# Kernel tuning notes

Measured on AMD Instinct MI355X. Metric: run time of the kernel, lower is better.

## Reference

```python
import jax, jax.numpy as jnp
import numpy as np
from jax import lax

BATCH = 1048576
NUM_DIGITS = 10


def _build_tables():
    # Exact replication of CarryAdderCell.__init__ table construction.
    next_carry = np.zeros((200, 2), dtype=np.float32)
    digit = np.zeros((200, 10), dtype=np.float32)
    for carry in (0, 1):
        for a in range(10):
            for b in range(10):
                idx = carry * 100 + a * 10 + b
                total = a + b + carry
                next_carry[idx, total // 10] = 1.0
                digit[idx, total % 10] = 1.0
    return jnp.asarray(digit), jnp.asarray(next_carry)


def setup_inputs() -> dict:
    key = jax.random.key(0)
    ka, kb = jax.random.split(key)
    a = jax.random.randint(ka, (BATCH, NUM_DIGITS), 0, 10, dtype=jnp.int32)
    b = jax.random.randint(kb, (BATCH, NUM_DIGITS), 0, 10, dtype=jnp.int32)
    digit_table, carry_table = _build_tables()
    return {"a": a, "b": b, "digit_table": digit_table, "carry_table": carry_table}


def reference(a, b, digit_table, carry_table):
    batch = a.shape[0]

    def step(carry_idx, ab):
        a_t, b_t = ab  # [batch] each
        table_idx = carry_idx * 100 + a_t * 10 + b_t  # [batch]
        digit_logits = digit_table[table_idx]          # [batch, 10]
        h_next = carry_table[table_idx]                # [batch, 2]
        next_carry = jnp.argmax(h_next, axis=-1).astype(jnp.int32)
        return next_carry, digit_logits

    # Process least-significant digit first (pos = num_digits-1 .. 0).
    xs = (a[:, ::-1].T, b[:, ::-1].T)  # each [num_digits, batch]
    carry0 = jnp.zeros((batch,), dtype=jnp.int32)  # initial one-hot carry -> argmax 0
    final_carry, logits_lsd = lax.scan(step, carry0, xs)
    # logits_lsd: [num_digits, batch, 10] in LSD-first order -> reverse, move batch first.
    result_10 = jnp.transpose(logits_lsd[::-1], (1, 0, 2))  # [batch, num_digits, 10]
    leading = jax.nn.one_hot(final_carry, 10, dtype=digit_table.dtype)[:, None, :]
    return jnp.concatenate([leading, result_10], axis=1)  # [batch, num_digits+1, 10]
```

## Files before the change

kernel.cpp:

```cpp
#include <hip/hip_runtime.h>


#define ROWS 128
#define THREADS 256
#define FPR 110

__global__ __launch_bounds__(THREADS) void adder_onehot_kernel(
    const int* __restrict__ a, const int* __restrict__ b,
    float* __restrict__ out, int batch) {
    __shared__ uint2 packed[ROWS + 1];

    const int t = threadIdx.x;
    const int row0 = blockIdx.x * ROWS;

    if (t < ROWS && row0 + t < batch) {
        const int* ap = a + (size_t)(row0 + t) * 10;
        const int* bp = b + (size_t)(row0 + t) * 10;
        int av[10], bv[10];
#pragma unroll
        for (int p = 0; p < 10; ++p) av[p] = ap[p];
#pragma unroll
        for (int p = 0; p < 10; ++p) bv[p] = bp[p];

        int dig[11];
        int carry = 0;
#pragma unroll
        for (int p = 9; p >= 0; --p) {
            int tot = av[p] + bv[p] + carry;
            int c = tot >= 10;
            dig[1 + p] = c ? tot - 10 : tot;
            carry = c;
        }
        dig[0] = carry;

        unsigned w0 = 0, w1 = 0;
#pragma unroll
        for (int pos = 0; pos < 8; ++pos) w0 |= (unsigned)dig[pos] << (4 * pos);
#pragma unroll
        for (int pos = 8; pos < 11; ++pos) w1 |= (unsigned)dig[pos] << (4 * (pos - 8));
        packed[t] = make_uint2(w0, w1);
    }
    __syncthreads();

    const int rows_here = min(ROWS, batch - row0);
    const int total_f = rows_here * FPR;
    const int nvec = total_f >> 2;
    float4* out4 = (float4*)(out + (size_t)row0 * FPR);

    int e0 = 4 * t;
    int row = e0 / 110;
    int rem = e0 - 110 * row;

    for (int i = t; i < nvec; i += THREADS) {
        uint2 p0 = packed[row];
        uint2 p1 = packed[row + 1];
        float4 v;
        float* vp = &v.x;
#pragma unroll
        for (int k = 0; k < 4; ++k) {
            int re = rem + k;
            bool wrap = re >= 110;
            int re2 = wrap ? re - 110 : re;
            unsigned wlo = wrap ? p1.x : p0.x;
            unsigned whi = wrap ? p1.y : p0.y;
            int pos = (re2 * 205) >> 11;
            int slot = re2 - 10 * pos;
            unsigned w = (pos >= 8) ? whi : wlo;
            int digit = (w >> ((pos & 7) * 4)) & 15;
            vp[k] = (digit == slot) ? 1.0f : 0.0f;
        }
        out4[i] = v;

        row += 9;
        rem += 34;
        if (rem >= 110) { rem -= 110; ++row; }
    }

    const int tail0 = nvec * 4;
    if (t < total_f - tail0) {
        int e = tail0 + t;
        int r = e / 110;
        int re2 = e - 110 * r;
        int pos = (re2 * 205) >> 11;
        int slot = re2 - 10 * pos;
        uint2 pw = packed[r];
        unsigned w = (pos >= 8) ? pw.y : pw.x;
        int digit = (w >> ((pos & 7) * 4)) & 15;
        out[(size_t)row0 * FPR + e] = (digit == slot) ? 1.0f : 0.0f;
    }
}

extern "C" void kernel_launch(void* const* d_in, const int* in_sizes, int n_in,
                              void* d_out, int out_size, void* d_ws, size_t ws_size,
                              hipStream_t stream) {
    const int* a = (const int*)d_in[0];
    const int* b = (const int*)d_in[1];
    float* out = (float*)d_out;
    const int batch = in_sizes[0] / 10;

    const int grid = (batch + ROWS - 1) / ROWS;
    adder_onehot_kernel<<<grid, THREADS, 0, stream>>>(a, b, out, batch);
}
```

Measured before the change: 112.7 us.

## Split adder into pack kernel and store kernel via workspace

Splits the work into two kernels. The first computes the packed digit words for every row and writes them to the workspace. The second reads the packed words and emits the one-hot float output, with 256 rows per block so all threads do useful work in the load phase. It also vectorises the input loads to int2, and keeps a fused fallback for when the workspace is too small. The split adds an extra launch and a round trip of 8 bytes per row through global memory, in exchange for removing the serial compute phase in which half of each block idled before the stores.

```diff
diff --git a/kernel.cpp b/kernel.cpp
--- a/kernel.cpp
+++ b/kernel.cpp
@@ -1,48 +1,60 @@
 #include <hip/hip_runtime.h>
 
 
-#define ROWS 128
 #define THREADS 256
 #define FPR 110
 
-__global__ __launch_bounds__(THREADS) void adder_onehot_kernel(
+__device__ __forceinline__ void compute_pack(const int* __restrict__ ap,
+                                             const int* __restrict__ bp,
+                                             unsigned& w0, unsigned& w1) {
+    int av[10], bv[10];
+    const int2* ap2 = (const int2*)ap;
+    const int2* bp2 = (const int2*)bp;
+#pragma unroll
+    for (int i = 0; i < 5; ++i) {
+        int2 va = ap2[i]; av[2*i] = va.x; av[2*i+1] = va.y;
+        int2 vb = bp2[i]; bv[2*i] = vb.x; bv[2*i+1] = vb.y;
+    }
+    int dig[11];
+    int carry = 0;
+#pragma unroll
+    for (int p = 9; p >= 0; --p) {
+        int tot = av[p] + bv[p] + carry;
+        int c = tot >= 10;
+        dig[1 + p] = c ? tot - 10 : tot;
+        carry = c;
+    }
+    dig[0] = carry;
+    w0 = 0; w1 = 0;
+#pragma unroll
+    for (int pos = 0; pos < 8; ++pos) w0 |= (unsigned)dig[pos] << (4 * pos);
+#pragma unroll
+    for (int pos = 8; pos < 11; ++pos) w1 |= (unsigned)dig[pos] << (4 * (pos - 8));
+}
+
+__global__ __launch_bounds__(THREADS) void adder_pack_kernel(
     const int* __restrict__ a, const int* __restrict__ b,
-    float* __restrict__ out, int batch) {
-    __shared__ uint2 packed[ROWS + 1];
+    uint2* __restrict__ ws, int batch) {
+    int r = blockIdx.x * THREADS + threadIdx.x;
+    if (r >= batch) return;
+    unsigned w0, w1;
+    compute_pack(a + (size_t)r * 10, b + (size_t)r * 10, w0, w1);
+    ws[r] = make_uint2(w0, w1);
+}
+
+#define BROWS 256
+__global__ __launch_bounds__(THREADS) void adder_store_kernel(
+    const uint2* __restrict__ ws, float* __restrict__ out, int batch) {
+    __shared__ uint2 packed[BROWS + 1];
 
     const int t = threadIdx.x;
-    const int row0 = blockIdx.x * ROWS;
+    const int row0 = blockIdx.x * BROWS;
+    const int rows_here = min(BROWS, batch - row0);
 
-    if (t < ROWS && row0 + t < batch) {
-        const int* ap = a + (size_t)(row0 + t) * 10;
-        const int* bp = b + (size_t)(row0 + t) * 10;
-        int av[10], bv[10];
-#pragma unroll
-        for (int p = 0; p < 10; ++p) av[p] = ap[p];
-#pragma unroll
-        for (int p = 0; p < 10; ++p) bv[p] = bp[p];
-
-        int dig[11];
-        int carry = 0;
-#pragma unroll
-        for (int p = 9; p >= 0; --p) {
-            int tot = av[p] + bv[p] + carry;
-            int c = tot >= 10;
-            dig[1 + p] = c ? tot - 10 : tot;
-            carry = c;
-        }
-        dig[0] = carry;
-
-        unsigned w0 = 0, w1 = 0;
-#pragma unroll
-        for (int pos = 0; pos < 8; ++pos) w0 |= (unsigned)dig[pos] << (4 * pos);
-#pragma unroll
-        for (int pos = 8; pos < 11; ++pos) w1 |= (unsigned)dig[pos] << (4 * (pos - 8));
-        packed[t] = make_uint2(w0, w1);
-    }
+    packed[t] = (t < rows_here) ? ws[row0 + t] : make_uint2(0u, 0u);
+    if (t == 0) packed[BROWS] = make_uint2(0u, 0u);
     __syncthreads();
 
-    const int rows_here = min(ROWS, batch - row0);
     const int total_f = rows_here * FPR;
     const int nvec = total_f >> 2;
     float4* out4 = (float4*)(out + (size_t)row0 * FPR);
@@ -90,6 +102,59 @@
     }
 }
 
+#define FROWS 128
+__global__ __launch_bounds__(THREADS) void adder_fused_kernel(
+    const int* __restrict__ a, const int* __restrict__ b,
+    float* __restrict__ out, int batch) {
+    __shared__ uint2 packed[FROWS + 1];
+    const int t = threadIdx.x;
+    const int row0 = blockIdx.x * FROWS;
+
+    if (t < FROWS) {
+        if (row0 + t < batch) {
+            unsigned w0, w1;
+            compute_pack(a + (size_t)(row0 + t) * 10, b + (size_t)(row0 + t) * 10, w0, w1);
+            packed[t] = make_uint2(w0, w1);
+        } else {
+            packed[t] = make_uint2(0u, 0u);
+        }
+    }
+    if (t == 0) packed[FROWS] = make_uint2(0u, 0u);
+    __syncthreads();
+
+    const int rows_here = min(FROWS, batch - row0);
+    const int total_f = rows_here * FPR;
+    const int nvec = total_f >> 2;
+    float4* out4 = (float4*)(out + (size_t)row0 * FPR);
+
+    int e0 = 4 * t;
+    int row = e0 / 110;
+    int rem = e0 - 110 * row;
+    for (int i = t; i < nvec; i += THREADS) {
+        uint2 p0 = packed[row];
+        uint2 p1 = packed[row + 1];
+        float4 v;
+        float* vp = &v.x;
+#pragma unroll
+        for (int k = 0; k < 4; ++k) {
+            int re = rem + k;
+            bool wrap = re >= 110;
+            int re2 = wrap ? re - 110 : re;
+            unsigned wlo = wrap ? p1.x : p0.x;
+            unsigned whi = wrap ? p1.y : p0.y;
+            int pos = (re2 * 205) >> 11;
+            int slot = re2 - 10 * pos;
+            unsigned w = (pos >= 8) ? whi : wlo;
+            int digit = (w >> ((pos & 7) * 4)) & 15;
+            vp[k] = (digit == slot) ? 1.0f : 0.0f;
+        }
+        out4[i] = v;
+        row += 9;
+        rem += 34;
+        if (rem >= 110) { rem -= 110; ++row; }
+    }
+}
+
 extern "C" void kernel_launch(void* const* d_in, const int* in_sizes, int n_in,
                               void* d_out, int out_size, void* d_ws, size_t ws_size,
                               hipStream_t stream) {
@@ -98,6 +163,14 @@
     float* out = (float*)d_out;
     const int batch = in_sizes[0] / 10;
 
-    const int grid = (batch + ROWS - 1) / ROWS;
-    adder_onehot_kernel<<<grid, THREADS, 0, stream>>>(a, b, out, batch);
+    const size_t need = (size_t)batch * sizeof(uint2);
+    if (ws_size >= need) {
+        const int gridA = (batch + THREADS - 1) / THREADS;
+        adder_pack_kernel<<<gridA, THREADS, 0, stream>>>(a, b, (uint2*)d_ws, batch);
+        const int gridB = (batch + BROWS - 1) / BROWS;
+        adder_store_kernel<<<gridB, THREADS, 0, stream>>>((const uint2*)d_ws, out, batch);
+    } else {
+        const int gridF = (batch + FROWS - 1) / FROWS;
+        adder_fused_kernel<<<gridF, THREADS, 0, stream>>>(a, b, out, batch);
+    }
 }
```

Result: slower. 117.3 us (+4.1%).
